# Optimization experiments

Measured on AMD Instinct MI355X. Metric: run time of the kernel, lower is better.

The kernel has to match this reference:

```python
import jax, jax.numpy as jnp
import numpy as np

N, T, H, D = 8, 192, 1024, 128
P = 4            # t_patch_size (kernel = stride)
TP = T // P      # 48 patch tokens
E = 16384
HOUR, WDAY = 48, 7


def conv1d_patch(e, W, b):
    # e: [B, Cin, T]; W: [Cout, Cin, P]; kernel == stride == P (non-overlapping)
    B, Ci, Tt = e.shape
    e = e.reshape(B, Ci, Tt // P, P)
    return jnp.einsum('bctk,ock->bot', e, W) + b[None, :, None]  # [B, Cout, T']


def gcn_propagate(x, src, dst, coef):
    # x: [B, H, D] ; symmetric-normalized sparse A_hat @ x
    msg = x[:, src, :] * coef[None, :, None]
    return jnp.zeros_like(x).at[:, dst, :].add(msg)


def setup_inputs() -> dict:
    key = jax.random.key(0)
    ks = jax.random.split(key, 12)
    x = jax.random.normal(ks[0], (N, 1, T, H, 1), dtype=jnp.float32)
    x_mark = jax.random.randint(ks[1], (N, T, 2), 0, 7).astype(jnp.int64)
    edges = jax.random.randint(ks[2], (E, 2), 0, H).astype(jnp.int64)
    node_split = jnp.arange(H, dtype=jnp.int64).reshape(4, 256)
    s = 0.02
    params = {
        'hour_emb': jax.random.normal(ks[3], (HOUR, D), jnp.float32) * s,
        'weekday_emb': jax.random.normal(ks[4], (WDAY, D), jnp.float32) * s,
        'timeconv_w': jax.random.normal(ks[5], (D, D, P), jnp.float32) * s,
        'timeconv_b': jnp.zeros((D,), jnp.float32),
        'tconv_w': jax.random.normal(ks[6], (D, 1, P), jnp.float32) * s,
        'tconv_b': jnp.zeros((D,), jnp.float32),
        'W1': jax.random.normal(ks[7], (D, D), jnp.float32) * s,
        'b1': jnp.zeros((D,), jnp.float32),
        'W2': jax.random.normal(ks[8], (D, D), jnp.float32) * s,
        'b2': jnp.zeros((D,), jnp.float32),
    }
    return dict(x=x, x_mark=x_mark, edges=edges, node_split=node_split, **params)


def reference(x, x_mark, edges, node_split, hour_emb, weekday_emb,
              timeconv_w, timeconv_b, tconv_w, tconv_b, W1, b1, W2, b2):
    # ---- TimeEmb (TemporalEmbedding, hour_num='48') ----
    hour_x = hour_emb[x_mark[:, :, 1]]        # [N, T, D]
    wday_x = weekday_emb[x_mark[:, :, 0]]     # [N, T, D]
    time_emb = conv1d_patch((hour_x + wday_x).transpose(0, 2, 1),
                            timeconv_w, timeconv_b).transpose(0, 2, 1)  # [N, T', D]

    # ---- temporal value embedding ----
    xv = jnp.squeeze(x, (1, 4)).transpose(0, 2, 1).reshape(N * H, 1, T)  # [N*H,1,T]
    tv = conv1d_patch(xv, tconv_w, tconv_b)                 # [N*H, D, T']
    tv = tv.transpose(0, 2, 1).reshape(N, H, TP, D)         # [N, H, T', D]
    tv = tv.transpose(0, 2, 1, 3).reshape(N * TP, H, D)     # [N*T', H, D]

    # ---- 2-layer GCN with self-loops + symmetric normalization ----
    src = jnp.concatenate([edges[:, 0], jnp.arange(H)])
    dst = jnp.concatenate([edges[:, 1], jnp.arange(H)])
    deg = jnp.zeros((H,), tv.dtype).at[dst].add(1.0)
    coef = jax.lax.rsqrt(deg[src] * deg[dst])
    h = jax.nn.relu(gcn_propagate(tv, src, dst, coef) @ W1 + b1)
    token = gcn_propagate(h, src, dst, coef) @ W2 + b2      # [N*T', H, D]
    token = token.reshape(N, TP, H, D)

    # ---- per-group gather + mean pooling, interleaved per time step ----
    G = node_split.shape[0]
    grouped = token[:, :, node_split.reshape(-1), :].reshape(N, TP, G, -1, D)
    token = grouped.mean(axis=3).reshape(N, TP * G, D)      # [N, T'*G, D]

    time_rep = jnp.repeat(time_emb, G, axis=1)              # [N, T'*G, D]
    out = token + time_rep  # is_time == 1; eval mode -> no dropout
    return out, time_rep
```

## Files before the change

kernel.cpp:

```cpp
#include <hip/hip_runtime.h>
#include <hip/hip_bf16.h>

#define NN 8
#define TT 192
#define HH 1024
#define DD 128
#define TPP 48
#define EE 16384
#define NEDGE (EE + HH)
#define BB (NN * TPP)
#define NOUT (NN * TT * DD)

typedef short bf16x8 __attribute__((ext_vector_type(8)));
typedef float f32x4 __attribute__((ext_vector_type(4)));

__device__ __forceinline__ float us2f(unsigned short u) {
  union { unsigned i; float f; } t;
  t.i = ((unsigned)u) << 16;
  return t.f;
}

__device__ __forceinline__ void acc6(float cf, unsigned u0, unsigned u1, unsigned u2,
                                     float& a0, float& a1, float& a2, float& a3,
                                     float& a4, float& a5) {
  union { unsigned i; float f; } lo, hi;
  lo.i = u0 << 16; hi.i = u0 & 0xffff0000u;
  a0 = fmaf(cf, lo.f, a0); a1 = fmaf(cf, hi.f, a1);
  lo.i = u1 << 16; hi.i = u1 & 0xffff0000u;
  a2 = fmaf(cf, lo.f, a2); a3 = fmaf(cf, hi.f, a3);
  lo.i = u2 << 16; hi.i = u2 & 0xffff0000u;
  a4 = fmaf(cf, lo.f, a4); a5 = fmaf(cf, hi.f, a5);
}

__global__ __launch_bounds__(256) void k_setup(
    const int* __restrict__ edges, const int* __restrict__ node_split,
    const float* __restrict__ x, __hip_bfloat16* __restrict__ Xall,
    const float* __restrict__ tcw, const float* __restrict__ tcb,
    const float* __restrict__ W1, float* __restrict__ CW,
    const float* __restrict__ W2, __hip_bfloat16* __restrict__ w2sw,
    int* __restrict__ fill, int* __restrict__ csr_src, float* __restrict__ csr_coef,
    float* __restrict__ csum, float* __restrict__ QT, int* __restrict__ row_ptr,
    const float* __restrict__ tw, float* __restrict__ twT) {
  __shared__ float tile[64][65];
  __shared__ int hist[1024];
  __shared__ int rp2[1024];
  __shared__ int invS[1024];
  __shared__ int wsumS[4];
  int tid = threadIdx.x, bid = blockIdx.x;
  if (bid < 384) {
    int i = bid * 256 + tid;
    if (i < 65536) twT[(i & 511) * DD + (i >> 9)] = tw[i];
    int tt = bid % 24, st = bid / 24;
    int t0 = tt * 64, s0 = st * 64;
    int sl = tid & 63, r4 = tid >> 6;
#pragma unroll 4
    for (int ii = 0; ii < 16; ++ii) {
      int tl = ii * 4 + r4;
      tile[tl][sl] = x[(size_t)(t0 + tl) * HH + s0 + sl];
    }
    __syncthreads();
#pragma unroll 4
    for (int ii = 0; ii < 16; ++ii) {
      int sl2 = ii * 4 + r4;
      Xall[(size_t)(s0 + sl2) * 1536 + t0 + sl] = __float2bfloat16(tile[sl][sl2]);
    }
  } else if (bid < 452) {
    int ex = (bid - 384) * 256 + tid;
    if (ex < 640) {
      int j = ex >> 7, o = ex & 127;
      float acc = 0.f;
      if (j < 4)
        for (int d = 0; d < DD; ++d) acc = fmaf(tcw[d * 4 + j], W1[d * DD + o], acc);
      else
        for (int d = 0; d < DD; ++d) acc = fmaf(tcb[d], W1[d * DD + o], acc);
      CW[j * DD + o] = acc;
    }
    int ew = ex - 1024;
    if (ew >= 0 && ew < 16384) {
      int n = ew >> 7, k = ew & 127;
      int dstb = n * 256 + (((k >> 3) ^ (n & 7)) * 16) + (k & 7) * 2;
      w2sw[dstb >> 1] = __float2bfloat16(W2[k * DD + n]);
    }
  } else {
    int lane = tid & 63, wid = tid >> 6;
    for (int i = tid; i < 1024; i += 256) hist[i] = 1;
    for (int i = tid; i < 1024; i += 256) invS[node_split[i]] = i;
    __syncthreads();
    for (int e = tid; e < EE; e += 256) atomicAdd(&hist[edges[2 * e + 1]], 1);
    __syncthreads();
    int4 d4 = ((const int4*)hist)[tid];
    int l0 = d4.x, l1 = d4.y, l2 = d4.z, l3 = d4.w;
    int lsum = l0 + l1 + l2 + l3;
    int incl = lsum;
#pragma unroll
    for (int off = 1; off < 64; off <<= 1) {
      int u = __shfl_up(incl, off, 64);
      if (lane >= off) incl += u;
    }
    if (lane == 63) wsumS[wid] = incl;
    __syncthreads();
    int base = 0;
    if (wid > 0) base += wsumS[0];
    if (wid > 1) base += wsumS[1];
    if (wid > 2) base += wsumS[2];
    int excl = base + incl - lsum;
    rp2[4 * tid] = excl;
    rp2[4 * tid + 1] = excl + l0;
    rp2[4 * tid + 2] = excl + l0 + l1;
    rp2[4 * tid + 3] = excl + l0 + l1 + l2;
    __syncthreads();
    if (bid == 452) {
      for (int i = tid; i < 1024; i += 256) row_ptr[i] = rp2[i];
      if (tid == 0) row_ptr[1024] = NEDGE;
    }
    int e = (bid - 452) * 256 + tid;
    int s, dt;
    if (e < EE) {
      int2 ed = ((const int2*)edges)[e];
      s = ed.x; dt = ed.y;
    } else {
      s = dt = e - EE;
    }
    float cf = rsqrtf((float)hist[s] * (float)hist[dt]);
    int pos = atomicAdd(&fill[dt], 1);
    int at = rp2[dt] + pos;
    csr_src[at] = s;
    csr_coef[at] = cf;
    atomicAdd(&csum[dt], cf);
    int g = invS[dt] >> 8;
    atomicAdd(&QT[s * 4 + g], cf * (1.0f / 256.0f));
  }
}

__global__ __launch_bounds__(256) void k_spmm(
    const int* __restrict__ row_ptr, const int* __restrict__ csr_src,
    const float* __restrict__ csr_coef, const __hip_bfloat16* __restrict__ Xall,
    __hip_bfloat16* __restrict__ xbar, const float* __restrict__ twT,
    const float* __restrict__ hour_emb, const float* __restrict__ wday_emb,
    float* __restrict__ UV) {
  __shared__ int sS[256];
  __shared__ float sC[256];
  int tid = threadIdx.x, bid = blockIdx.x;
  if (bid >= HH) {
    int i = (bid - HH) * 256 + tid;
    if (i < 24576) {
      int o = i & 127, r = i >> 7;
      int hr = r % 48, k = r / 48;
      float acc = 0.f;
      for (int d = 0; d < DD; ++d)
        acc = fmaf(twT[(d * 4 + k) * DD + o], hour_emb[hr * DD + d], acc);
      UV[i] = acc;
    } else if (i < 28160) {
      int j = i - 24576;
      int o = j & 127, r = j >> 7;
      int wd = r % 7, k = r / 7;
      float acc = 0.f;
      for (int d = 0; d < DD; ++d)
        acc = fmaf(twT[(d * 4 + k) * DD + o], wday_emb[wd * DD + d], acc);
      UV[i] = acc;
    }
    return;
  }
  int h = bid;
  int j0 = row_ptr[h], j1 = row_ptr[h + 1];
  int cnt = j1 - j0;
  int cs = cnt < 256 ? cnt : 256;
  if (tid < cs) { sS[tid] = csr_src[j0 + tid]; sC[tid] = csr_coef[j0 + tid]; }
  __syncthreads();
  float a0 = 0.f, a1 = 0.f, a2 = 0.f, a3 = 0.f, a4 = 0.f, a5 = 0.f;
  int j = 0;
  for (; j + 4 <= cs; j += 4) {
    const unsigned* x0 = (const unsigned*)(Xall + (size_t)sS[j] * 1536);
    const unsigned* x1 = (const unsigned*)(Xall + (size_t)sS[j + 1] * 1536);
    const unsigned* x2 = (const unsigned*)(Xall + (size_t)sS[j + 2] * 1536);
    const unsigned* x3 = (const unsigned*)(Xall + (size_t)sS[j + 3] * 1536);
    unsigned u00 = x0[tid], u01 = x0[tid + 256], u02 = x0[tid + 512];
    unsigned u10 = x1[tid], u11 = x1[tid + 256], u12 = x1[tid + 512];
    unsigned u20 = x2[tid], u21 = x2[tid + 256], u22 = x2[tid + 512];
    unsigned u30 = x3[tid], u31 = x3[tid + 256], u32 = x3[tid + 512];
    float c0 = sC[j], c1 = sC[j + 1], c2 = sC[j + 2], c3 = sC[j + 3];
    acc6(c0, u00, u01, u02, a0, a1, a2, a3, a4, a5);
    acc6(c1, u10, u11, u12, a0, a1, a2, a3, a4, a5);
    acc6(c2, u20, u21, u22, a0, a1, a2, a3, a4, a5);
    acc6(c3, u30, u31, u32, a0, a1, a2, a3, a4, a5);
  }
  for (; j < cs; ++j) {
    const unsigned* xr = (const unsigned*)(Xall + (size_t)sS[j] * 1536);
    unsigned u0 = xr[tid], u1 = xr[tid + 256], u2 = xr[tid + 512];
    acc6(sC[j], u0, u1, u2, a0, a1, a2, a3, a4, a5);
  }
  for (; j < cnt; ++j) {
    int s = csr_src[j0 + j];
    float cf = csr_coef[j0 + j];
    const unsigned* xr = (const unsigned*)(Xall + (size_t)s * 1536);
    unsigned u0 = xr[tid], u1 = xr[tid + 256], u2 = xr[tid + 512];
    acc6(cf, u0, u1, u2, a0, a1, a2, a3, a4, a5);
  }
  unsigned* xw = (unsigned*)(xbar + (size_t)h * 1536);
  union { __hip_bfloat16 h2[2]; unsigned u; } pk;
  pk.h2[0] = __float2bfloat16(a0); pk.h2[1] = __float2bfloat16(a1);
  xw[tid] = pk.u;
  pk.h2[0] = __float2bfloat16(a2); pk.h2[1] = __float2bfloat16(a3);
  xw[tid + 256] = pk.u;
  pk.h2[0] = __float2bfloat16(a4); pk.h2[1] = __float2bfloat16(a5);
  xw[tid + 512] = pk.u;
}

__global__ __launch_bounds__(256) void k_red(const __hip_bfloat16* __restrict__ xbar,
                                             const float* __restrict__ csum,
                                             const float* __restrict__ QT,
                                             const float* __restrict__ CW,
                                             const float* __restrict__ b1,
                                             float* __restrict__ ypar,
                                             const int* __restrict__ xm,
                                             const float* __restrict__ tcb,
                                             const float* __restrict__ UV,
                                             float* __restrict__ out) {
  __shared__ float4 xb4[256];
  __shared__ float4 qv[256];
  __shared__ float csv[256];
  __shared__ float yL[512];
  int tid = threadIdx.x, bid = blockIdx.x;
  if (bid >= 1536) {
    int bb = bid - 1536;
    int half = tid >> 7, o = tid & 127;
    int b = bb * 2 + half;
    int n = b / TPP, tp = b % TPP;
    const float* U = UV;
    const float* V = UV + 24576;
    float acc = tcb[o];
#pragma unroll
    for (int k = 0; k < 4; ++k) {
      int t = tp * 4 + k;
      int wd = xm[(n * TT + t) * 2 + 0];
      int hr = xm[(n * TT + t) * 2 + 1];
      acc += U[k * 6144 + hr * DD + o] + V[k * 896 + wd * DD + o];
    }
    size_t base = (size_t)NOUT + ((size_t)n * TT + tp * 4) * DD + o;
    out[base] = acc;
    out[base + DD] = acc;
    out[base + 2 * DD] = acc;
    out[base + 3 * DD] = acc;
    return;
  }
  int b = bid >> 2, qt = bid & 3;
  if (tid < 128) {
    for (int r = tid; r < 256; r += 128) {
      int h = qt * 256 + r;
      ushort4 us = *(const ushort4*)(xbar + (size_t)h * 1536 + b * 4);
      xb4[r] = make_float4(us2f(us.x), us2f(us.y), us2f(us.z), us2f(us.w));
      qv[r] = *(const float4*)(QT + h * 4);
      csv[r] = csum[h];
    }
  }
  int lane = tid & 63, w = tid >> 6;
  if (tid < 128) {
    int o0 = lane, o1 = lane + 64;
    float cw0a = CW[o0], cw1a = CW[DD + o0], cw2a = CW[2 * DD + o0];
    float cw3a = CW[3 * DD + o0], cw4a = CW[4 * DD + o0];
    float cw0b = CW[o1], cw1b = CW[DD + o1], cw2b = CW[2 * DD + o1];
    float cw3b = CW[3 * DD + o1], cw4b = CW[4 * DD + o1];
    float b1a = b1[o0], b1b = b1[o1];
    __syncthreads();
    float y0a = 0.f, y1a = 0.f, y2a = 0.f, y3a = 0.f;
    float y0b = 0.f, y1b = 0.f, y2b = 0.f, y3b = 0.f;
    int h0 = w * 128;
#pragma unroll 4
    for (int hh = h0; hh < h0 + 128; ++hh) {
      float4 xv = xb4[hh];
      float4 q = qv[hh];
      float c = csv[hh];
      float t0 = fmaf(c, cw4a, b1a);
      t0 = fmaf(xv.x, cw0a, t0);
      t0 = fmaf(xv.y, cw1a, t0);
      t0 = fmaf(xv.z, cw2a, t0);
      t0 = fmaf(xv.w, cw3a, t0);
      t0 = fmaxf(t0, 0.f);
      float t1 = fmaf(c, cw4b, b1b);
      t1 = fmaf(xv.x, cw0b, t1);
      t1 = fmaf(xv.y, cw1b, t1);
      t1 = fmaf(xv.z, cw2b, t1);
      t1 = fmaf(xv.w, cw3b, t1);
      t1 = fmaxf(t1, 0.f);
      y0a = fmaf(q.x, t0, y0a); y1a = fmaf(q.y, t0, y1a);
      y2a = fmaf(q.z, t0, y2a); y3a = fmaf(q.w, t0, y3a);
      y0b = fmaf(q.x, t1, y0b); y1b = fmaf(q.y, t1, y1b);
      y2b = fmaf(q.z, t1, y2b); y3b = fmaf(q.w, t1, y3b);
    }
    if (w == 0) {
      yL[o0] = y0a; yL[128 + o0] = y1a; yL[256 + o0] = y2a; yL[384 + o0] = y3a;
      yL[o1] = y0b; yL[128 + o1] = y1b; yL[256 + o1] = y2b; yL[384 + o1] = y3b;
    }
    __syncthreads();
    if (w == 1) {
      yL[o0] += y0a; yL[128 + o0] += y1a; yL[256 + o0] += y2a; yL[384 + o0] += y3a;
      yL[o1] += y0b; yL[128 + o1] += y1b; yL[256 + o1] += y2b; yL[384 + o1] += y3b;
    }
    __syncthreads();
    float* yp = ypar + ((size_t)qt * BB + b) * 512;
    for (int i = tid; i < 512; i += 128) yp[i] = yL[i];
  } else {
    __syncthreads();
    __syncthreads();
    __syncthreads();
  }
}

__global__ __launch_bounds__(256, 2) void k_out(const float* __restrict__ ypar,
                                                const __hip_bfloat16* __restrict__ w2sw,
                                                const float* __restrict__ b2,
                                                float* __restrict__ out) {
  __shared__ __align__(16) char Wr[32768];
  __shared__ __align__(16) char Gr[16384];
  int tid = threadIdx.x;
  int m0 = blockIdx.x * 64;
  {
    const uint4* ws = (const uint4*)w2sw;
    uint4* wd = (uint4*)Wr;
    for (int i = tid; i < 2048; i += 256) wd[i] = ws[i];
  }
#pragma unroll 4
  for (int it = 0; it < 16; ++it) {
    int pi = it * 256 + tid;
    int row = pi >> 6, kp = pi & 63;
    int base = (m0 + row) * 128 + 2 * kp;
    float s0 = 0.f, s1 = 0.f;
#pragma unroll
    for (int p = 0; p < 4; ++p) {
      s0 += ypar[(size_t)p * (BB * 512) + base];
      s1 += ypar[(size_t)p * (BB * 512) + base + 1];
    }
    union { __hip_bfloat16 h[2]; unsigned u; } pk;
    pk.h[0] = __float2bfloat16(s0);
    pk.h[1] = __float2bfloat16(s1);
    *(unsigned*)(Gr + row * 256 + (((kp >> 2) ^ (row & 7)) * 16) + (kp & 3) * 4) = pk.u;
  }
  int lane = tid & 63, w = tid >> 6;
  int colq = lane & 15, quad = lane >> 4;
  float bo[8];
#pragma unroll
  for (int jn = 0; jn < 8; ++jn) bo[jn] = b2[jn * 16 + colq];
  __syncthreads();

  f32x4 acc[8];
#pragma unroll
  for (int jn = 0; jn < 8; ++jn) acc[jn] = (f32x4){0.f, 0.f, 0.f, 0.f};
  int arow = w * 16 + colq;
#pragma unroll
  for (int kc = 0; kc < 4; ++kc) {
    bf16x8 af = *(const bf16x8*)(Gr + arow * 256 + (((kc * 4 + quad) ^ (arow & 7)) * 16));
#pragma unroll
    for (int jn = 0; jn < 8; ++jn) {
      int nr = jn * 16 + colq;
      bf16x8 bf = *(const bf16x8*)(Wr + nr * 256 + (((kc * 4 + quad) ^ (nr & 7)) * 16));
      acc[jn] = __builtin_amdgcn_mfma_f32_16x16x32_bf16(af, bf, acc[jn], 0, 0, 0);
    }
  }
#pragma unroll
  for (int reg = 0; reg < 4; ++reg) {
    int m = m0 + w * 16 + quad * 4 + reg;
    int b = m >> 2, g = m & 3;
    int n_ = b / TPP, tp = b % TPP;
    size_t rb = ((size_t)(n_ * TT + tp * 4 + g)) * DD;
#pragma unroll
    for (int jn = 0; jn < 8; ++jn) {
      int o = jn * 16 + colq;
      out[rb + o] = acc[jn][reg] + bo[jn] + out[(size_t)NOUT + rb + o];
    }
  }
}

extern "C" void kernel_launch(void* const* d_in, const int* in_sizes, int n_in,
                              void* d_out, int out_size, void* d_ws, size_t ws_size,
                              hipStream_t stream) {
  const float* x = (const float*)d_in[0];
  const int* xm = (const int*)d_in[1];
  const int* edges = (const int*)d_in[2];
  const int* node_split = (const int*)d_in[3];
  const float* hour_emb = (const float*)d_in[4];
  const float* wday_emb = (const float*)d_in[5];
  const float* timeconv_w = (const float*)d_in[6];
  const float* timeconv_b = (const float*)d_in[7];
  const float* tcw = (const float*)d_in[8];
  const float* tcb = (const float*)d_in[9];
  const float* W1 = (const float*)d_in[10];
  const float* b1 = (const float*)d_in[11];
  const float* W2 = (const float*)d_in[12];
  const float* b2 = (const float*)d_in[13];
  float* out = (float*)d_out;

  char* w = (char*)d_ws;
  int* fill = (int*)(w + 4096);
  float* csum = (float*)(w + 8192);
  float* QT = (float*)(w + 12288);
  int* row_ptr = (int*)(w + 28672);
  int* csr_src = (int*)(w + 37120);
  float* csr_coef = (float*)(w + 106752);
  __hip_bfloat16* w2sw = (__hip_bfloat16*)(w + 176384);
  float* CW = (float*)(w + 209152);
  float* twT = (float*)(w + 213248);
  __hip_bfloat16* Xall = (__hip_bfloat16*)(w + 475392);
  float* ypar = (float*)(w + 475392);
  __hip_bfloat16* xbar = (__hip_bfloat16*)(w + 3621120);
  float* UV = (float*)(w + 6766848);

  hipMemsetAsync(w + 4096, 0, 24576, stream);
  k_setup<<<520, 256, 0, stream>>>(edges, node_split, x, Xall, tcw, tcb, W1, CW, W2,
                                   w2sw, fill, csr_src, csr_coef, csum, QT, row_ptr,
                                   timeconv_w, twT);
  k_spmm<<<HH + 110, 256, 0, stream>>>(row_ptr, csr_src, csr_coef, Xall, xbar, twT,
                                       hour_emb, wday_emb, UV);
  k_red<<<1536 + 192, 256, 0, stream>>>(xbar, csum, QT, CW, b1, ypar, xm, tcb, UV,
                                        out);
  k_out<<<24, 256, 0, stream>>>(ypar, w2sw, b2, out);
}
```

Before: 145.3 us.

## Build CSR in a single block with shared-memory atomics and drop memset

The CSR scatter, per-node coefficient sums and group-pooling weights were previously built by 68 redundant blocks that each recomputed the degree histogram and then did global atomics. A single block now processes all edges with shared-memory atomics and writes csum/QT/row_ptr once, which removes the workspace memset. k_spmm moves its small UV precompute blocks to the front of the grid. k_red drops to 128-thread blocks because half the threads were idle. The trade-off is that the CSR build becomes a serial single-block loop over about 17K edges, which may sit on the critical path.

```diff
diff --git a/kernel.cpp b/kernel.cpp
--- a/kernel.cpp
+++ b/kernel.cpp
@@ -38,13 +38,16 @@
     const float* __restrict__ tcw, const float* __restrict__ tcb,
     const float* __restrict__ W1, float* __restrict__ CW,
     const float* __restrict__ W2, __hip_bfloat16* __restrict__ w2sw,
-    int* __restrict__ fill, int* __restrict__ csr_src, float* __restrict__ csr_coef,
+    int* __restrict__ csr_src, float* __restrict__ csr_coef,
     float* __restrict__ csum, float* __restrict__ QT, int* __restrict__ row_ptr,
     const float* __restrict__ tw, float* __restrict__ twT) {
   __shared__ float tile[64][65];
   __shared__ int hist[1024];
   __shared__ int rp2[1024];
   __shared__ int invS[1024];
+  __shared__ int fillS[1024];
+  __shared__ float csumS[1024];
+  __shared__ float QTS[4096];
   __shared__ int wsumS[4];
   int tid = threadIdx.x, bid = blockIdx.x;
   if (bid < 384) {
@@ -83,8 +86,13 @@
     }
   } else {
     int lane = tid & 63, wid = tid >> 6;
-    for (int i = tid; i < 1024; i += 256) hist[i] = 1;
-    for (int i = tid; i < 1024; i += 256) invS[node_split[i]] = i;
+    for (int i = tid; i < 1024; i += 256) {
+      hist[i] = 1;
+      invS[node_split[i]] = i;
+      fillS[i] = 0;
+      csumS[i] = 0.f;
+    }
+    for (int i = tid; i < 4096; i += 256) QTS[i] = 0.f;
     __syncthreads();
     for (int e = tid; e < EE; e += 256) atomicAdd(&hist[edges[2 * e + 1]], 1);
     __syncthreads();
@@ -109,26 +117,30 @@
     rp2[4 * tid + 2] = excl + l0 + l1;
     rp2[4 * tid + 3] = excl + l0 + l1 + l2;
     __syncthreads();
-    if (bid == 452) {
-      for (int i = tid; i < 1024; i += 256) row_ptr[i] = rp2[i];
-      if (tid == 0) row_ptr[1024] = NEDGE;
-    }
-    int e = (bid - 452) * 256 + tid;
-    int s, dt;
-    if (e < EE) {
-      int2 ed = ((const int2*)edges)[e];
-      s = ed.x; dt = ed.y;
-    } else {
-      s = dt = e - EE;
-    }
-    float cf = rsqrtf((float)hist[s] * (float)hist[dt]);
-    int pos = atomicAdd(&fill[dt], 1);
-    int at = rp2[dt] + pos;
-    csr_src[at] = s;
-    csr_coef[at] = cf;
-    atomicAdd(&csum[dt], cf);
-    int g = invS[dt] >> 8;
-    atomicAdd(&QT[s * 4 + g], cf * (1.0f / 256.0f));
+    for (int e = tid; e < NEDGE; e += 256) {
+      int s, dt;
+      if (e < EE) {
+        int2 ed = ((const int2*)edges)[e];
+        s = ed.x; dt = ed.y;
+      } else {
+        s = dt = e - EE;
+      }
+      float cf = rsqrtf((float)hist[s] * (float)hist[dt]);
+      int pos = atomicAdd(&fillS[dt], 1);
+      int at = rp2[dt] + pos;
+      csr_src[at] = s;
+      csr_coef[at] = cf;
+      atomicAdd(&csumS[dt], cf);
+      int g = invS[dt] >> 8;
+      atomicAdd(&QTS[s * 4 + g], cf * (1.0f / 256.0f));
+    }
+    __syncthreads();
+    for (int i = tid; i < 1024; i += 256) {
+      row_ptr[i] = rp2[i];
+      csum[i] = csumS[i];
+    }
+    for (int i = tid; i < 4096; i += 256) QT[i] = QTS[i];
+    if (tid == 0) row_ptr[1024] = NEDGE;
   }
 }
 
@@ -141,8 +153,8 @@
   __shared__ int sS[256];
   __shared__ float sC[256];
   int tid = threadIdx.x, bid = blockIdx.x;
-  if (bid >= HH) {
-    int i = (bid - HH) * 256 + tid;
+  if (bid < 110) {
+    int i = bid * 256 + tid;
     if (i < 24576) {
       int o = i & 127, r = i >> 7;
       int hr = r % 48, k = r / 48;
@@ -161,7 +173,7 @@
     }
     return;
   }
-  int h = bid;
+  int h = bid - 110;
   int j0 = row_ptr[h], j1 = row_ptr[h + 1];
   int cnt = j1 - j0;
   int cs = cnt < 256 ? cnt : 256;
@@ -206,7 +218,7 @@
   xw[tid + 512] = pk.u;
 }
 
-__global__ __launch_bounds__(256) void k_red(const __hip_bfloat16* __restrict__ xbar,
+__global__ __launch_bounds__(128) void k_red(const __hip_bfloat16* __restrict__ xbar,
                                              const float* __restrict__ csum,
                                              const float* __restrict__ QT,
                                              const float* __restrict__ CW,
@@ -222,19 +234,16 @@
   __shared__ float yL[512];
   int tid = threadIdx.x, bid = blockIdx.x;
   if (bid >= 1536) {
-    int bb = bid - 1536;
-    int half = tid >> 7, o = tid & 127;
-    int b = bb * 2 + half;
+    int b = bid - 1536;
     int n = b / TPP, tp = b % TPP;
-    const float* U = UV;
-    const float* V = UV + 24576;
+    int o = tid;
     float acc = tcb[o];
 #pragma unroll
     for (int k = 0; k < 4; ++k) {
       int t = tp * 4 + k;
       int wd = xm[(n * TT + t) * 2 + 0];
       int hr = xm[(n * TT + t) * 2 + 1];
-      acc += U[k * 6144 + hr * DD + o] + V[k * 896 + wd * DD + o];
+      acc += UV[k * 6144 + hr * DD + o] + UV[24576 + k * 896 + wd * DD + o];
     }
     size_t base = (size_t)NOUT + ((size_t)n * TT + tp * 4) * DD + o;
     out[base] = acc;
@@ -244,66 +253,58 @@
     return;
   }
   int b = bid >> 2, qt = bid & 3;
-  if (tid < 128) {
-    for (int r = tid; r < 256; r += 128) {
-      int h = qt * 256 + r;
-      ushort4 us = *(const ushort4*)(xbar + (size_t)h * 1536 + b * 4);
-      xb4[r] = make_float4(us2f(us.x), us2f(us.y), us2f(us.z), us2f(us.w));
-      qv[r] = *(const float4*)(QT + h * 4);
-      csv[r] = csum[h];
-    }
+  for (int r = tid; r < 256; r += 128) {
+    int h = qt * 256 + r;
+    ushort4 us = *(const ushort4*)(xbar + (size_t)h * 1536 + b * 4);
+    xb4[r] = make_float4(us2f(us.x), us2f(us.y), us2f(us.z), us2f(us.w));
+    qv[r] = *(const float4*)(QT + h * 4);
+    csv[r] = csum[h];
   }
   int lane = tid & 63, w = tid >> 6;
-  if (tid < 128) {
-    int o0 = lane, o1 = lane + 64;
-    float cw0a = CW[o0], cw1a = CW[DD + o0], cw2a = CW[2 * DD + o0];
-    float cw3a = CW[3 * DD + o0], cw4a = CW[4 * DD + o0];
-    float cw0b = CW[o1], cw1b = CW[DD + o1], cw2b = CW[2 * DD + o1];
-    float cw3b = CW[3 * DD + o1], cw4b = CW[4 * DD + o1];
-    float b1a = b1[o0], b1b = b1[o1];
-    __syncthreads();
-    float y0a = 0.f, y1a = 0.f, y2a = 0.f, y3a = 0.f;
-    float y0b = 0.f, y1b = 0.f, y2b = 0.f, y3b = 0.f;
-    int h0 = w * 128;
+  int o0 = lane, o1 = lane + 64;
+  float cw0a = CW[o0], cw1a = CW[DD + o0], cw2a = CW[2 * DD + o0];
+  float cw3a = CW[3 * DD + o0], cw4a = CW[4 * DD + o0];
+  float cw0b = CW[o1], cw1b = CW[DD + o1], cw2b = CW[2 * DD + o1];
+  float cw3b = CW[3 * DD + o1], cw4b = CW[4 * DD + o1];
+  float b1a = b1[o0], b1b = b1[o1];
+  __syncthreads();
+  float y0a = 0.f, y1a = 0.f, y2a = 0.f, y3a = 0.f;
+  float y0b = 0.f, y1b = 0.f, y2b = 0.f, y3b = 0.f;
+  int h0 = w * 128;
 #pragma unroll 4
-    for (int hh = h0; hh < h0 + 128; ++hh) {
-      float4 xv = xb4[hh];
-      float4 q = qv[hh];
-      float c = csv[hh];
-      float t0 = fmaf(c, cw4a, b1a);
-      t0 = fmaf(xv.x, cw0a, t0);
-      t0 = fmaf(xv.y, cw1a, t0);
-      t0 = fmaf(xv.z, cw2a, t0);
-      t0 = fmaf(xv.w, cw3a, t0);
-      t0 = fmaxf(t0, 0.f);
-      float t1 = fmaf(c, cw4b, b1b);
-      t1 = fmaf(xv.x, cw0b, t1);
-      t1 = fmaf(xv.y, cw1b, t1);
-      t1 = fmaf(xv.z, cw2b, t1);
-      t1 = fmaf(xv.w, cw3b, t1);
-      t1 = fmaxf(t1, 0.f);
-      y0a = fmaf(q.x, t0, y0a); y1a = fmaf(q.y, t0, y1a);
-      y2a = fmaf(q.z, t0, y2a); y3a = fmaf(q.w, t0, y3a);
-      y0b = fmaf(q.x, t1, y0b); y1b = fmaf(q.y, t1, y1b);
-      y2b = fmaf(q.z, t1, y2b); y3b = fmaf(q.w, t1, y3b);
-    }
-    if (w == 0) {
-      yL[o0] = y0a; yL[128 + o0] = y1a; yL[256 + o0] = y2a; yL[384 + o0] = y3a;
-      yL[o1] = y0b; yL[128 + o1] = y1b; yL[256 + o1] = y2b; yL[384 + o1] = y3b;
-    }
-    __syncthreads();
-    if (w == 1) {
-      yL[o0] += y0a; yL[128 + o0] += y1a; yL[256 + o0] += y2a; yL[384 + o0] += y3a;
-      yL[o1] += y0b; yL[128 + o1] += y1b; yL[256 + o1] += y2b; yL[384 + o1] += y3b;
-    }
-    __syncthreads();
-    float* yp = ypar + ((size_t)qt * BB + b) * 512;
-    for (int i = tid; i < 512; i += 128) yp[i] = yL[i];
-  } else {
-    __syncthreads();
-    __syncthreads();
-    __syncthreads();
-  }
+  for (int hh = h0; hh < h0 + 128; ++hh) {
+    float4 xv = xb4[hh];
+    float4 q = qv[hh];
+    float c = csv[hh];
+    float t0 = fmaf(c, cw4a, b1a);
+    t0 = fmaf(xv.x, cw0a, t0);
+    t0 = fmaf(xv.y, cw1a, t0);
+    t0 = fmaf(xv.z, cw2a, t0);
+    t0 = fmaf(xv.w, cw3a, t0);
+    t0 = fmaxf(t0, 0.f);
+    float t1 = fmaf(c, cw4b, b1b);
+    t1 = fmaf(xv.x, cw0b, t1);
+    t1 = fmaf(xv.y, cw1b, t1);
+    t1 = fmaf(xv.z, cw2b, t1);
+    t1 = fmaf(xv.w, cw3b, t1);
+    t1 = fmaxf(t1, 0.f);
+    y0a = fmaf(q.x, t0, y0a); y1a = fmaf(q.y, t0, y1a);
+    y2a = fmaf(q.z, t0, y2a); y3a = fmaf(q.w, t0, y3a);
+    y0b = fmaf(q.x, t1, y0b); y1b = fmaf(q.y, t1, y1b);
+    y2b = fmaf(q.z, t1, y2b); y3b = fmaf(q.w, t1, y3b);
+  }
+  if (w == 0) {
+    yL[o0] = y0a; yL[128 + o0] = y1a; yL[256 + o0] = y2a; yL[384 + o0] = y3a;
+    yL[o1] = y0b; yL[128 + o1] = y1b; yL[256 + o1] = y2b; yL[384 + o1] = y3b;
+  }
+  __syncthreads();
+  if (w == 1) {
+    yL[o0] += y0a; yL[128 + o0] += y1a; yL[256 + o0] += y2a; yL[384 + o0] += y3a;
+    yL[o1] += y0b; yL[128 + o1] += y1b; yL[256 + o1] += y2b; yL[384 + o1] += y3b;
+  }
+  __syncthreads();
+  float* yp = ypar + ((size_t)qt * BB + b) * 512;
+  for (int i = tid; i < 512; i += 128) yp[i] = yL[i];
 }
 
 __global__ __launch_bounds__(256, 2) void k_out(const float* __restrict__ ypar,
@@ -390,7 +391,6 @@
   float* out = (float*)d_out;
 
   char* w = (char*)d_ws;
-  int* fill = (int*)(w + 4096);
   float* csum = (float*)(w + 8192);
   float* QT = (float*)(w + 12288);
   int* row_ptr = (int*)(w + 28672);
@@ -404,13 +404,12 @@
   __hip_bfloat16* xbar = (__hip_bfloat16*)(w + 3621120);
   float* UV = (float*)(w + 6766848);
 
-  hipMemsetAsync(w + 4096, 0, 24576, stream);
-  k_setup<<<520, 256, 0, stream>>>(edges, node_split, x, Xall, tcw, tcb, W1, CW, W2,
-                                   w2sw, fill, csr_src, csr_coef, csum, QT, row_ptr,
+  k_setup<<<453, 256, 0, stream>>>(edges, node_split, x, Xall, tcw, tcb, W1, CW, W2,
+                                   w2sw, csr_src, csr_coef, csum, QT, row_ptr,
                                    timeconv_w, twT);
-  k_spmm<<<HH + 110, 256, 0, stream>>>(row_ptr, csr_src, csr_coef, Xall, xbar, twT,
+  k_spmm<<<110 + HH, 256, 0, stream>>>(row_ptr, csr_src, csr_coef, Xall, xbar, twT,
                                        hour_emb, wday_emb, UV);
-  k_red<<<1536 + 192, 256, 0, stream>>>(xbar, csum, QT, CW, b1, ypar, xm, tcb, UV,
-                                        out);
+  k_red<<<1536 + BB, 128, 0, stream>>>(xbar, csum, QT, CW, b1, ypar, xm, tcb, UV,
+                                       out);
   k_out<<<24, 256, 0, stream>>>(ypar, w2sw, b2, out);
 }
```

New measurement: 186.6 us. 1.28x slower.
